# Performance work log

Hardware: AMD Instinct MI355X
Metric: run time of the kernel (lower is better)

The kernel has to match this reference:

```python
import jax, jax.numpy as jnp
import numpy as np

N = 50000      # nodes
E = 800000     # unique directed edges (avg degree 16)
F = 64         # input_dim
D = 64         # output_dim (== F -> residual is identity)
ALPHA = 0.5
LCS_THR = 0.5  # enable_lcs_masking=True, lcs_threshold=0.5


def setup_inputs() -> dict:
    key = jax.random.key(0)
    ks = jax.random.split(key, 16)
    x = jax.random.normal(ks[0], (N, F), jnp.float32)
    src = jax.random.randint(ks[1], (E,), 0, N, jnp.int32)
    dst = jax.random.randint(ks[2], (E,), 0, N, jnp.int32)
    # integer-valued multiplicities in {1,2,3,4} (recurring-transaction counts)
    counts = jnp.floor(jax.random.uniform(ks[3], (E,), jnp.float32) * 4.0) + 1.0
    def lin(k, fan_in, shape):
        return jax.random.normal(k, shape, jnp.float32) / np.float32(np.sqrt(fan_in))
    return dict(
        x=x, counts=counts,
        W_s2d=lin(ks[4], F, (F, D)), b_s2d=jnp.zeros((D,), jnp.float32),
        W_d2s=lin(ks[5], F, (F, D)), b_d2s=jnp.zeros((D,), jnp.float32),
        W_l1=lin(ks[6], 2 * F, (2 * F, F)), b_l1=jnp.zeros((F,), jnp.float32),
        W_l2=lin(ks[7], F, (F, 1)), b_l2=jnp.zeros((1,), jnp.float32),
        W_g1=lin(ks[8], 2 * D, (2 * D, D)), b_g1=jnp.zeros((D,), jnp.float32),
        W_g2=lin(ks[9], D, (D, 1)), b_g2=jnp.zeros((1,), jnp.float32),
        src=src, dst=dst,
    )


def reference(x, counts, W_s2d, b_s2d, W_d2s, b_d2s,
              W_l1, b_l1, W_l2, b_l2, W_g1, b_g1, W_g2, b_g2,
              src, dst):
    # in/out degrees from full (unmasked) multiplicities, clamped at 1
    in_deg = jnp.maximum(jax.ops.segment_sum(counts, dst, num_segments=N), 1.0)
    out_deg = jnp.maximum(jax.ops.segment_sum(counts, src, num_segments=N), 1.0)

    # LCS per unique edge: sigmoid(MLP([x_src, x_dst])), detached in torch
    lcs_in = jnp.concatenate([x[src], x[dst]], axis=-1)          # [E, 2F]
    lcs = jax.nn.sigmoid(
        jax.nn.relu(lcs_in @ W_l1 + b_l1) @ W_l2 + b_l2)[:, 0]   # [E]
    lcs = jax.lax.stop_gradient(lcs)
    keep = (lcs >= LCS_THR).astype(x.dtype)                      # LCS masking

    # symmetric-normalized edge weights with multiplicity counts
    w = counts * keep * jax.lax.rsqrt(out_deg[src] * in_deg[dst])  # [E]

    # direction-aware message passing (redundancy-eliminated, per unique edge)
    h_s2d = x @ W_s2d + b_s2d                                    # [N, D]
    h_d2s = x @ W_d2s + b_d2s                                    # [N, D]
    m_in = jax.ops.segment_sum(w[:, None] * h_s2d[src], dst, num_segments=N)
    m_out = jax.ops.segment_sum(w[:, None] * h_d2s[dst], src, num_segments=N)

    # node-wise gating over inbound vs outbound flows
    gate = jax.nn.sigmoid(
        jax.nn.relu(jnp.concatenate([m_in, m_out], axis=-1) @ W_g1 + b_g1)
        @ W_g2 + b_g2)                                           # [N, 1]

    # gated alpha-blend + identity residual (input_dim == output_dim)
    out = ALPHA * gate * m_in + (1.0 - ALPHA) * (1.0 - gate) * m_out + x
    return out
```

## Files before the change

kernel.cpp:

```cpp
#include <hip/hip_runtime.h>
#include <math.h>


typedef unsigned long long u64;

#define SLOTS 56

__device__ __forceinline__ float bflo(unsigned u) { return __uint_as_float(u << 16); }
__device__ __forceinline__ float bfhi(unsigned u) { return __uint_as_float(u & 0xffff0000u); }
__device__ __forceinline__ unsigned rne16(float f) {
    unsigned u = __float_as_uint(f);
    return (u + 0x7fffu + ((u >> 16) & 1u)) >> 16;
}

__global__ __launch_bounds__(256) void proj_zero_kernel(
    const float* __restrict__ x,
    const float* __restrict__ Wl1,  const float* __restrict__ bl1,
    const float* __restrict__ Ws2d, const float* __restrict__ bs2d,
    const float* __restrict__ Wd2s, const float* __restrict__ bd2s,
    const float* __restrict__ Wg1,  float* __restrict__ Wg1q,
    float* __restrict__ A, float* __restrict__ B,
    unsigned* __restrict__ Ah, unsigned* __restrict__ Bh,
    unsigned* __restrict__ HSh, unsigned* __restrict__ HDh,
    int4* __restrict__ zp4, int nz4, int PB, int N)
{
    if (blockIdx.x >= PB) {
        if (blockIdx.x == PB + 64) {
            for (int i = threadIdx.x; i < 8192; i += 256) {
                const int k = i >> 6, c = i & 63;
                Wg1q[((k >> 2) * 64 + c) * 4 + (k & 3)] = Wg1[i];
            }
            return;
        }
        const int t0 = (blockIdx.x - PB) * 256 + threadIdx.x;
        const int stride = 64 * 256;
        const int4 z = make_int4(0, 0, 0, 0);
        for (int i = t0; i < nz4; i += stride) zp4[i] = z;
        return;
    }
    __shared__ float xs[64][64];
    const int tid  = threadIdx.x;
    const int n0   = blockIdx.x * 64;
    const int wv   = tid >> 6;
    const int cc   = tid & 63;
    const int side = wv & 1;
    const int par  = wv >> 1;

    const float* W0 = side ? (Wl1 + 64 * 64) : Wl1;
    const float* W1 = side ? Wd2s : Ws2d;
    const float  b0 = side ? 0.f : bl1[cc];
    const float  b1 = side ? bd2s[cc] : bs2d[cc];
    float*    oA  = side ? B  : A;
    unsigned* oAh = side ? Bh : Ah;
    unsigned* oH  = side ? HDh : HSh;

    float w0[64], w1[64];
#pragma unroll
    for (int k = 0; k < 64; ++k) {
        w0[k] = W0[k * 64 + cc];
        w1[k] = W1[k * 64 + cc];
    }

#pragma unroll
    for (int j = 0; j < 4; ++j) {
        int f4  = tid + j * 256;
        int row = f4 >> 4;
        int c4  = f4 & 15;
        int gn  = n0 + row;
        float4 v = (gn < N) ? ((const float4*)x)[(long)gn * 16 + c4]
                            : make_float4(0.f, 0.f, 0.f, 0.f);
        ((float4*)&xs[row][0])[c4] = v;
    }
    __syncthreads();

    const int nmax = (N - n0 < 64) ? (N - n0) : 64;
    for (int n = par; n < nmax; n += 2) {
        float a0 = b0, a1 = b1;
#pragma unroll
        for (int k = 0; k < 64; k += 4) {
            float4 xv = *((const float4*)&xs[n][k]);
            a0 += xv.x * w0[k] + xv.y * w0[k + 1] + xv.z * w0[k + 2] + xv.w * w0[k + 3];
            a1 += xv.x * w1[k] + xv.y * w1[k + 1] + xv.z * w1[k + 2] + xv.w * w1[k + 3];
        }
        const long gn = n0 + n;
        oA[gn * 64 + cc] = a0;
        const float p0 = __shfl_xor(a0, 1);
        const float p1 = __shfl_xor(a1, 1);
        if ((cc & 1) == 0) {
            oAh[gn * 32 + (cc >> 1)] = (rne16(p0) << 16) | rne16(a0);
            oH [gn * 32 + (cc >> 1)] = (rne16(p1) << 16) | rne16(a1);
        }
    }
}

#define LCS_MARGIN 0.04f
__global__ __launch_bounds__(256) void edge_w_kernel(
    const int* __restrict__ src, const int* __restrict__ dst,
    const float* __restrict__ counts,
    const float* __restrict__ A, const float* __restrict__ B,
    const unsigned* __restrict__ Ah, const unsigned* __restrict__ Bh,
    const float* __restrict__ Wl2, const float* __restrict__ bl2,
    u64* __restrict__ pk, unsigned* __restrict__ rec, int N, int E)
{
    const int tid = threadIdx.x;
    const int e   = blockIdx.x * 32 + (tid >> 3);
    const int c   = tid & 7;
    if (e >= E) return;

    const int s = src[e];
    const int d = dst[e];
    const uint4  ua  = *((const uint4*)(Ah + (long)s * 32 + c * 4));
    const uint4  ub  = *((const uint4*)(Bh + (long)d * 32 + c * 4));
    const float4 wl0 = *((const float4*)(Wl2 + c * 8));
    const float4 wl1 = *((const float4*)(Wl2 + c * 8 + 4));

    float p = fmaxf(bflo(ua.x) + bflo(ub.x), 0.f) * wl0.x
            + fmaxf(bfhi(ua.x) + bfhi(ub.x), 0.f) * wl0.y
            + fmaxf(bflo(ua.y) + bflo(ub.y), 0.f) * wl0.z
            + fmaxf(bfhi(ua.y) + bfhi(ub.y), 0.f) * wl0.w
            + fmaxf(bflo(ua.z) + bflo(ub.z), 0.f) * wl1.x
            + fmaxf(bfhi(ua.z) + bfhi(ub.z), 0.f) * wl1.y
            + fmaxf(bflo(ua.w) + bflo(ub.w), 0.f) * wl1.z
            + fmaxf(bfhi(ua.w) + bfhi(ub.w), 0.f) * wl1.w;
    p += __shfl_xor(p, 1); p += __shfl_xor(p, 2); p += __shfl_xor(p, 4);

    float z = p + bl2[0];
    if (fabsf(z) < LCS_MARGIN) {
        const float4 a0 = *((const float4*)(A + (long)s * 64 + c * 8));
        const float4 a1 = *((const float4*)(A + (long)s * 64 + c * 8 + 4));
        const float4 b0 = *((const float4*)(B + (long)d * 64 + c * 8));
        const float4 b1 = *((const float4*)(B + (long)d * 64 + c * 8 + 4));
        float q = fmaxf(a0.x + b0.x, 0.f) * wl0.x + fmaxf(a0.y + b0.y, 0.f) * wl0.y
                + fmaxf(a0.z + b0.z, 0.f) * wl0.z + fmaxf(a0.w + b0.w, 0.f) * wl0.w
                + fmaxf(a1.x + b1.x, 0.f) * wl1.x + fmaxf(a1.y + b1.y, 0.f) * wl1.y
                + fmaxf(a1.z + b1.z, 0.f) * wl1.z + fmaxf(a1.w + b1.w, 0.f) * wl1.w;
        q += __shfl_xor(q, 1); q += __shfl_xor(q, 2); q += __shfl_xor(q, 4);
        z = q + bl2[0];
    }

    if (c == 0) {
        const u64 keep = (z >= 0.f) ? 1ull : 0ull;
        const unsigned ic = (unsigned)__float2int_rn(counts[e]);
        const u64 od = atomicAdd(pk + d,     (keep << 32) | (u64)ic);
        const u64 os = atomicAdd(pk + N + s, (keep << 32) | (u64)ic);
        if (keep) {
            rec[(long)d * SLOTS + (int)(od >> 32)]       = ((unsigned)s << 16) | ic;
            rec[(long)(N + s) * SLOTS + (int)(os >> 32)] = ((unsigned)d << 16) | ic;
        }
    }
}

__global__ __launch_bounds__(256) void gather_gate_kernel(
    const u64* __restrict__ pk, const unsigned* __restrict__ rec,
    const unsigned* __restrict__ HSh, const unsigned* __restrict__ HDh,
    const float* __restrict__ x,
    const float* __restrict__ Wg1q, const float* __restrict__ bg1,
    const float* __restrict__ Wg2, const float* __restrict__ bg2,
    float* __restrict__ out, int N)
{
    __shared__ float mbuf[16][128];
    const int tid  = threadIdx.x;
    const int wv   = tid >> 6;
    const int lane = tid & 63;
    const int g    = lane >> 3;
    const int c    = lane & 7;
    const int nb   = blockIdx.x * 16 + wv * 4;

    const unsigned* pklo = (const unsigned*)pk;

    for (int j = 0; j < 4; ++j) {
        const int n   = nb + j;
        const int row = wv * 4 + j;
        if (n >= N) {
            if (g == 0) {
#pragma unroll
                for (int q = 0; q < 8; ++q) {
                    mbuf[row][c * 8 + q]      = 0.f;
                    mbuf[row][64 + c * 8 + q] = 0.f;
                }
            }
            continue;
        }

        const u64 pin  = pk[n];
        const u64 pout = pk[N + n];
        const int ei = (int)(pin >> 32);
        const int eo = (int)(pout >> 32);
        const float qin  = 1.f / sqrtf(fmaxf((float)(unsigned)pin,  1.f));
        const float qout = 1.f / sqrtf(fmaxf((float)(unsigned)pout, 1.f));
        const unsigned* rin  = rec + (long)n * SLOTS;
        const unsigned* rout = rec + (long)(N + n) * SLOTS;

        float mi[8], mo[8];
#pragma unroll
        for (int q = 0; q < 8; ++q) { mi[q] = 0.f; mo[q] = 0.f; }

        int ii = g, jo = g;
        while ((ii < ei) || (jo < eo)) {
            const bool pa = ii < ei;
            const bool pb = jo < eo;
            const unsigned ra = rin[pa ? ii : 0];
            const unsigned rb = rout[pb ? jo : 0];
            const unsigned sa = ra >> 16;
            const unsigned sb = rb >> 16;
            const float dga = (float)pklo[2 * (N + (int)sa)];
            const float dgb = (float)pklo[2 * (int)sb];
            const float wa = pa ? (float)(ra & 0xFFu) * (1.f / sqrtf(fmaxf(dga, 1.f))) : 0.f;
            const float wb = pb ? (float)(rb & 0xFFu) * (1.f / sqrtf(fmaxf(dgb, 1.f))) : 0.f;
            const uint4 ua = *((const uint4*)(HSh + (long)sa * 32 + c * 4));
            const uint4 ub = *((const uint4*)(HDh + (long)sb * 32 + c * 4));
            mi[0] += wa * bflo(ua.x);  mo[0] += wb * bflo(ub.x);
            mi[1] += wa * bfhi(ua.x);  mo[1] += wb * bfhi(ub.x);
            mi[2] += wa * bflo(ua.y);  mo[2] += wb * bflo(ub.y);
            mi[3] += wa * bfhi(ua.y);  mo[3] += wb * bfhi(ub.y);
            mi[4] += wa * bflo(ua.z);  mo[4] += wb * bflo(ub.z);
            mi[5] += wa * bfhi(ua.z);  mo[5] += wb * bfhi(ub.z);
            mi[6] += wa * bflo(ua.w);  mo[6] += wb * bflo(ub.w);
            mi[7] += wa * bfhi(ua.w);  mo[7] += wb * bfhi(ub.w);
            ii += 8; jo += 8;
        }

#pragma unroll
        for (int q = 0; q < 8; ++q) {
            mi[q] += __shfl_xor(mi[q], 8);
            mi[q] += __shfl_xor(mi[q], 16);
            mi[q] += __shfl_xor(mi[q], 32);
            mo[q] += __shfl_xor(mo[q], 8);
            mo[q] += __shfl_xor(mo[q], 16);
            mo[q] += __shfl_xor(mo[q], 32);
        }
        if (g == 0) {
#pragma unroll
            for (int q = 0; q < 8; ++q) {
                mbuf[row][c * 8 + q]      = mi[q] * qin;
                mbuf[row][64 + c * 8 + q] = mo[q] * qout;
            }
        }
    }

    const float bgv = bg1[lane];
    float ac0 = bgv, ac1 = bgv, ac2 = bgv, ac3 = bgv;
    const float* m0 = &mbuf[wv * 4 + 0][0];
    const float* m1 = &mbuf[wv * 4 + 1][0];
    const float* m2 = &mbuf[wv * 4 + 2][0];
    const float* m3 = &mbuf[wv * 4 + 3][0];
#pragma unroll 4
    for (int k4 = 0; k4 < 32; ++k4) {
        const float4 w4 = ((const float4*)Wg1q)[k4 * 64 + lane];
        const float4 q0 = ((const float4*)m0)[k4];
        const float4 q1 = ((const float4*)m1)[k4];
        const float4 q2 = ((const float4*)m2)[k4];
        const float4 q3 = ((const float4*)m3)[k4];
        ac0 += q0.x * w4.x + q0.y * w4.y + q0.z * w4.z + q0.w * w4.w;
        ac1 += q1.x * w4.x + q1.y * w4.y + q1.z * w4.z + q1.w * w4.w;
        ac2 += q2.x * w4.x + q2.y * w4.y + q2.z * w4.z + q2.w * w4.w;
        ac3 += q3.x * w4.x + q3.y * w4.y + q3.z * w4.z + q3.w * w4.w;
    }
    const float wg2 = Wg2[lane];
    float v0 = fmaxf(ac0, 0.f) * wg2;
    float v1 = fmaxf(ac1, 0.f) * wg2;
    float v2 = fmaxf(ac2, 0.f) * wg2;
    float v3 = fmaxf(ac3, 0.f) * wg2;
#pragma unroll
    for (int m = 1; m <= 32; m <<= 1) {
        v0 += __shfl_xor(v0, m);
        v1 += __shfl_xor(v1, m);
        v2 += __shfl_xor(v2, m);
        v3 += __shfl_xor(v3, m);
    }
    const float bb = bg2[0];
    float gt[4];
    gt[0] = 1.f / (1.f + expf(-(v0 + bb)));
    gt[1] = 1.f / (1.f + expf(-(v1 + bb)));
    gt[2] = 1.f / (1.f + expf(-(v2 + bb)));
    gt[3] = 1.f / (1.f + expf(-(v3 + bb)));

#pragma unroll
    for (int j = 0; j < 4; ++j) {
        const int n = nb + j;
        if (n >= N) continue;
        const float miv = mbuf[wv * 4 + j][lane];
        const float mov = mbuf[wv * 4 + j][64 + lane];
        out[(long)n * 64 + lane] = 0.5f * gt[j] * miv + 0.5f * (1.f - gt[j]) * mov
                                 + x[(long)n * 64 + lane];
    }
}

extern "C" void kernel_launch(void* const* d_in, const int* in_sizes, int n_in,
                              void* d_out, int out_size, void* d_ws, size_t ws_size,
                              hipStream_t stream) {
    const float* x      = (const float*)d_in[0];
    const float* counts = (const float*)d_in[1];
    const float* Ws2d   = (const float*)d_in[2];
    const float* bs2d   = (const float*)d_in[3];
    const float* Wd2s   = (const float*)d_in[4];
    const float* bd2s   = (const float*)d_in[5];
    const float* Wl1    = (const float*)d_in[6];
    const float* bl1    = (const float*)d_in[7];
    const float* Wl2    = (const float*)d_in[8];
    const float* bl2    = (const float*)d_in[9];
    const float* Wg1    = (const float*)d_in[10];
    const float* bg1    = (const float*)d_in[11];
    const float* Wg2    = (const float*)d_in[12];
    const float* bg2    = (const float*)d_in[13];
    const int*   src    = (const int*)d_in[14];
    const int*   dst    = (const int*)d_in[15];

    const int N  = in_sizes[0] / 64;
    const int E  = in_sizes[14];
    const int PB = (N + 63) / 64;

    float* ws      = (float*)d_ws;
    float* Wg1q    = ws;
    float* A       = ws + 8192;
    float* B       = A + 64L * N;
    unsigned* Ah   = (unsigned*)(B + 64L * N);
    unsigned* Bh   = Ah + 32L * N;
    unsigned* HSh  = Bh + 32L * N;
    unsigned* HDh  = HSh + 32L * N;
    u64* pk        = (u64*)(HDh + 32L * N);
    unsigned* rec  = (unsigned*)(pk + 2L * N);

    proj_zero_kernel<<<PB + 65, 256, 0, stream>>>(
        x, Wl1, bl1, Ws2d, bs2d, Wd2s, bd2s, Wg1, Wg1q,
        A, B, Ah, Bh, HSh, HDh, (int4*)pk, N, PB, N);

    edge_w_kernel<<<(E + 31) / 32, 256, 0, stream>>>(
        src, dst, counts, A, B, Ah, Bh, Wl2, bl2, pk, rec, N, E);

    gather_gate_kernel<<<(N + 15) / 16, 256, 0, stream>>>(
        pk, rec, HSh, HDh, x, Wg1q, bg1, Wg2, bg2, (float*)d_out, N);
}
```

Before: 277.0 us.

## Fuse three kernels into persistent cooperative megakernel and overlap HS/HD projection with edge pass

Replaces the three launches with one persistent cooperative kernel that uses grid-wide syncs between phases. The HS/HD message projection moves out of the first phase and is interleaved with the edge-scoring tiles, so it overlaps that latency-bound pass. Register weight arrays are halved per tile. Costs: grid syncs, a fixed 1024-block grid under a 4-blocks-per-CU launch bound, and extra x reloads for the second projection pass.

```diff
diff --git a/kernel.cpp b/kernel.cpp
--- a/kernel.cpp
+++ b/kernel.cpp
@@ -1,10 +1,14 @@
 #include <hip/hip_runtime.h>
+#include <hip/hip_cooperative_groups.h>
 #include <math.h>
 
+namespace cg = cooperative_groups;
+
 
 typedef unsigned long long u64;
 
 #define SLOTS 56
+#define LCS_MARGIN 0.04f
 
 __device__ __forceinline__ float bflo(unsigned u) { return __uint_as_float(u << 16); }
 __device__ __forceinline__ float bfhi(unsigned u) { return __uint_as_float(u & 0xffff0000u); }
@@ -13,53 +17,48 @@
     return (u + 0x7fffu + ((u >> 16) & 1u)) >> 16;
 }
 
-__global__ __launch_bounds__(256) void proj_zero_kernel(
-    const float* __restrict__ x,
-    const float* __restrict__ Wl1,  const float* __restrict__ bl1,
-    const float* __restrict__ Ws2d, const float* __restrict__ bs2d,
-    const float* __restrict__ Wd2s, const float* __restrict__ bd2s,
-    const float* __restrict__ Wg1,  float* __restrict__ Wg1q,
-    float* __restrict__ A, float* __restrict__ B,
-    unsigned* __restrict__ Ah, unsigned* __restrict__ Bh,
-    unsigned* __restrict__ HSh, unsigned* __restrict__ HDh,
-    int4* __restrict__ zp4, int nz4, int PB, int N)
+union __align__(16) SMem {
+    float xs[64][64];
+    float mbuf[16][128];
+};
+
+struct MArgs {
+    const float* x; const float* counts;
+    const float* Ws2d; const float* bs2d; const float* Wd2s; const float* bd2s;
+    const float* Wl1;  const float* bl1;  const float* Wl2;  const float* bl2;
+    const float* Wg1;  const float* bg1;  const float* Wg2;  const float* bg2;
+    const int* src; const int* dst;
+    float* Wg1q; float* A; float* B;
+    unsigned* Ah; unsigned* Bh; unsigned* HSh; unsigned* HDh;
+    u64* pk; unsigned* rec; float* out;
+    int PB, EB, GB, N, E, nz4;
+    int mode;
+};
+
+template <bool ABPHASE>
+__device__ __forceinline__ void proj_tile(const MArgs& a, int b, int tid, SMem& sm)
 {
-    if (blockIdx.x >= PB) {
-        if (blockIdx.x == PB + 64) {
-            for (int i = threadIdx.x; i < 8192; i += 256) {
-                const int k = i >> 6, c = i & 63;
-                Wg1q[((k >> 2) * 64 + c) * 4 + (k & 3)] = Wg1[i];
-            }
-            return;
-        }
-        const int t0 = (blockIdx.x - PB) * 256 + threadIdx.x;
-        const int stride = 64 * 256;
-        const int4 z = make_int4(0, 0, 0, 0);
-        for (int i = t0; i < nz4; i += stride) zp4[i] = z;
-        return;
-    }
-    __shared__ float xs[64][64];
-    const int tid  = threadIdx.x;
-    const int n0   = blockIdx.x * 64;
+    const int n0   = b * 64;
     const int wv   = tid >> 6;
     const int cc   = tid & 63;
     const int side = wv & 1;
     const int par  = wv >> 1;
 
-    const float* W0 = side ? (Wl1 + 64 * 64) : Wl1;
-    const float* W1 = side ? Wd2s : Ws2d;
-    const float  b0 = side ? 0.f : bl1[cc];
-    const float  b1 = side ? bd2s[cc] : bs2d[cc];
-    float*    oA  = side ? B  : A;
-    unsigned* oAh = side ? Bh : Ah;
-    unsigned* oH  = side ? HDh : HSh;
-
-    float w0[64], w1[64];
-#pragma unroll
-    for (int k = 0; k < 64; ++k) {
-        w0[k] = W0[k * 64 + cc];
-        w1[k] = W1[k * 64 + cc];
-    }
+    const float* W; float bv; float* oA = nullptr; unsigned* oP;
+    if (ABPHASE) {
+        W  = side ? (a.Wl1 + 64 * 64) : a.Wl1;
+        bv = side ? 0.f : a.bl1[cc];
+        oA = side ? a.B  : a.A;
+        oP = side ? a.Bh : a.Ah;
+    } else {
+        W  = side ? a.Wd2s : a.Ws2d;
+        bv = side ? a.bd2s[cc] : a.bs2d[cc];
+        oP = side ? a.HDh : a.HSh;
+    }
+
+    float w[64];
+#pragma unroll
+    for (int k = 0; k < 64; ++k) w[k] = W[k * 64 + cc];
 
 #pragma unroll
     for (int j = 0; j < 4; ++j) {
@@ -67,52 +66,41 @@
         int row = f4 >> 4;
         int c4  = f4 & 15;
         int gn  = n0 + row;
-        float4 v = (gn < N) ? ((const float4*)x)[(long)gn * 16 + c4]
-                            : make_float4(0.f, 0.f, 0.f, 0.f);
-        ((float4*)&xs[row][0])[c4] = v;
+        float4 v = (gn < a.N) ? ((const float4*)a.x)[(long)gn * 16 + c4]
+                              : make_float4(0.f, 0.f, 0.f, 0.f);
+        ((float4*)&sm.xs[row][0])[c4] = v;
     }
     __syncthreads();
 
-    const int nmax = (N - n0 < 64) ? (N - n0) : 64;
+    const int nmax = (a.N - n0 < 64) ? (a.N - n0) : 64;
     for (int n = par; n < nmax; n += 2) {
-        float a0 = b0, a1 = b1;
+        float acc = bv;
 #pragma unroll
         for (int k = 0; k < 64; k += 4) {
-            float4 xv = *((const float4*)&xs[n][k]);
-            a0 += xv.x * w0[k] + xv.y * w0[k + 1] + xv.z * w0[k + 2] + xv.w * w0[k + 3];
-            a1 += xv.x * w1[k] + xv.y * w1[k + 1] + xv.z * w1[k + 2] + xv.w * w1[k + 3];
+            float4 xv = *((const float4*)&sm.xs[n][k]);
+            acc += xv.x * w[k] + xv.y * w[k + 1] + xv.z * w[k + 2] + xv.w * w[k + 3];
         }
         const long gn = n0 + n;
-        oA[gn * 64 + cc] = a0;
-        const float p0 = __shfl_xor(a0, 1);
-        const float p1 = __shfl_xor(a1, 1);
-        if ((cc & 1) == 0) {
-            oAh[gn * 32 + (cc >> 1)] = (rne16(p0) << 16) | rne16(a0);
-            oH [gn * 32 + (cc >> 1)] = (rne16(p1) << 16) | rne16(a1);
-        }
-    }
-}
-
-#define LCS_MARGIN 0.04f
-__global__ __launch_bounds__(256) void edge_w_kernel(
-    const int* __restrict__ src, const int* __restrict__ dst,
-    const float* __restrict__ counts,
-    const float* __restrict__ A, const float* __restrict__ B,
-    const unsigned* __restrict__ Ah, const unsigned* __restrict__ Bh,
-    const float* __restrict__ Wl2, const float* __restrict__ bl2,
-    u64* __restrict__ pk, unsigned* __restrict__ rec, int N, int E)
+        if (ABPHASE) oA[gn * 64 + cc] = acc;
+        const float p = __shfl_xor(acc, 1);
+        if ((cc & 1) == 0)
+            oP[gn * 32 + (cc >> 1)] = (rne16(p) << 16) | rne16(acc);
+    }
+    __syncthreads();
+}
+
+__device__ __forceinline__ void edge_tile(const MArgs& a, int b, int tid)
 {
-    const int tid = threadIdx.x;
-    const int e   = blockIdx.x * 32 + (tid >> 3);
-    const int c   = tid & 7;
-    if (e >= E) return;
-
-    const int s = src[e];
-    const int d = dst[e];
-    const uint4  ua  = *((const uint4*)(Ah + (long)s * 32 + c * 4));
-    const uint4  ub  = *((const uint4*)(Bh + (long)d * 32 + c * 4));
-    const float4 wl0 = *((const float4*)(Wl2 + c * 8));
-    const float4 wl1 = *((const float4*)(Wl2 + c * 8 + 4));
+    const int e = b * 32 + (tid >> 3);
+    const int c = tid & 7;
+    if (e >= a.E) return;
+
+    const int s = a.src[e];
+    const int d = a.dst[e];
+    const uint4  ua  = *((const uint4*)(a.Ah + (long)s * 32 + c * 4));
+    const uint4  ub  = *((const uint4*)(a.Bh + (long)d * 32 + c * 4));
+    const float4 wl0 = *((const float4*)(a.Wl2 + c * 8));
+    const float4 wl1 = *((const float4*)(a.Wl2 + c * 8 + 4));
 
     float p = fmaxf(bflo(ua.x) + bflo(ub.x), 0.f) * wl0.x
             + fmaxf(bfhi(ua.x) + bfhi(ub.x), 0.f) * wl0.y
@@ -124,49 +112,42 @@
             + fmaxf(bfhi(ua.w) + bfhi(ub.w), 0.f) * wl1.w;
     p += __shfl_xor(p, 1); p += __shfl_xor(p, 2); p += __shfl_xor(p, 4);
 
-    float z = p + bl2[0];
+    float z = p + a.bl2[0];
     if (fabsf(z) < LCS_MARGIN) {
-        const float4 a0 = *((const float4*)(A + (long)s * 64 + c * 8));
-        const float4 a1 = *((const float4*)(A + (long)s * 64 + c * 8 + 4));
-        const float4 b0 = *((const float4*)(B + (long)d * 64 + c * 8));
-        const float4 b1 = *((const float4*)(B + (long)d * 64 + c * 8 + 4));
+        const float4 a0 = *((const float4*)(a.A + (long)s * 64 + c * 8));
+        const float4 a1 = *((const float4*)(a.A + (long)s * 64 + c * 8 + 4));
+        const float4 b0 = *((const float4*)(a.B + (long)d * 64 + c * 8));
+        const float4 b1 = *((const float4*)(a.B + (long)d * 64 + c * 8 + 4));
         float q = fmaxf(a0.x + b0.x, 0.f) * wl0.x + fmaxf(a0.y + b0.y, 0.f) * wl0.y
                 + fmaxf(a0.z + b0.z, 0.f) * wl0.z + fmaxf(a0.w + b0.w, 0.f) * wl0.w
                 + fmaxf(a1.x + b1.x, 0.f) * wl1.x + fmaxf(a1.y + b1.y, 0.f) * wl1.y
                 + fmaxf(a1.z + b1.z, 0.f) * wl1.z + fmaxf(a1.w + b1.w, 0.f) * wl1.w;
         q += __shfl_xor(q, 1); q += __shfl_xor(q, 2); q += __shfl_xor(q, 4);
-        z = q + bl2[0];
+        z = q + a.bl2[0];
     }
 
     if (c == 0) {
         const u64 keep = (z >= 0.f) ? 1ull : 0ull;
-        const unsigned ic = (unsigned)__float2int_rn(counts[e]);
-        const u64 od = atomicAdd(pk + d,     (keep << 32) | (u64)ic);
-        const u64 os = atomicAdd(pk + N + s, (keep << 32) | (u64)ic);
+        const unsigned ic = (unsigned)__float2int_rn(a.counts[e]);
+        const u64 od = atomicAdd(a.pk + d,       (keep << 32) | (u64)ic);
+        const u64 os = atomicAdd(a.pk + a.N + s, (keep << 32) | (u64)ic);
         if (keep) {
-            rec[(long)d * SLOTS + (int)(od >> 32)]       = ((unsigned)s << 16) | ic;
-            rec[(long)(N + s) * SLOTS + (int)(os >> 32)] = ((unsigned)d << 16) | ic;
-        }
-    }
-}
-
-__global__ __launch_bounds__(256) void gather_gate_kernel(
-    const u64* __restrict__ pk, const unsigned* __restrict__ rec,
-    const unsigned* __restrict__ HSh, const unsigned* __restrict__ HDh,
-    const float* __restrict__ x,
-    const float* __restrict__ Wg1q, const float* __restrict__ bg1,
-    const float* __restrict__ Wg2, const float* __restrict__ bg2,
-    float* __restrict__ out, int N)
+            a.rec[(long)d * SLOTS + (int)(od >> 32)]         = ((unsigned)s << 16) | ic;
+            a.rec[(long)(a.N + s) * SLOTS + (int)(os >> 32)] = ((unsigned)d << 16) | ic;
+        }
+    }
+}
+
+__device__ __forceinline__ void gather_tile(const MArgs& a, int b, int tid, SMem& sm)
 {
-    __shared__ float mbuf[16][128];
-    const int tid  = threadIdx.x;
     const int wv   = tid >> 6;
     const int lane = tid & 63;
     const int g    = lane >> 3;
     const int c    = lane & 7;
-    const int nb   = blockIdx.x * 16 + wv * 4;
-
-    const unsigned* pklo = (const unsigned*)pk;
+    const int nb   = b * 16 + wv * 4;
+    const int N    = a.N;
+
+    const unsigned* pklo = (const unsigned*)a.pk;
 
     for (int j = 0; j < 4; ++j) {
         const int n   = nb + j;
@@ -175,21 +156,21 @@
             if (g == 0) {
 #pragma unroll
                 for (int q = 0; q < 8; ++q) {
-                    mbuf[row][c * 8 + q]      = 0.f;
-                    mbuf[row][64 + c * 8 + q] = 0.f;
+                    sm.mbuf[row][c * 8 + q]      = 0.f;
+                    sm.mbuf[row][64 + c * 8 + q] = 0.f;
                 }
             }
             continue;
         }
 
-        const u64 pin  = pk[n];
-        const u64 pout = pk[N + n];
+        const u64 pin  = a.pk[n];
+        const u64 pout = a.pk[N + n];
         const int ei = (int)(pin >> 32);
         const int eo = (int)(pout >> 32);
         const float qin  = 1.f / sqrtf(fmaxf((float)(unsigned)pin,  1.f));
         const float qout = 1.f / sqrtf(fmaxf((float)(unsigned)pout, 1.f));
-        const unsigned* rin  = rec + (long)n * SLOTS;
-        const unsigned* rout = rec + (long)(N + n) * SLOTS;
+        const unsigned* rin  = a.rec + (long)n * SLOTS;
+        const unsigned* rout = a.rec + (long)(N + n) * SLOTS;
 
         float mi[8], mo[8];
 #pragma unroll
@@ -207,8 +188,8 @@
             const float dgb = (float)pklo[2 * (int)sb];
             const float wa = pa ? (float)(ra & 0xFFu) * (1.f / sqrtf(fmaxf(dga, 1.f))) : 0.f;
             const float wb = pb ? (float)(rb & 0xFFu) * (1.f / sqrtf(fmaxf(dgb, 1.f))) : 0.f;
-            const uint4 ua = *((const uint4*)(HSh + (long)sa * 32 + c * 4));
-            const uint4 ub = *((const uint4*)(HDh + (long)sb * 32 + c * 4));
+            const uint4 ua = *((const uint4*)(a.HSh + (long)sa * 32 + c * 4));
+            const uint4 ub = *((const uint4*)(a.HDh + (long)sb * 32 + c * 4));
             mi[0] += wa * bflo(ua.x);  mo[0] += wb * bflo(ub.x);
             mi[1] += wa * bfhi(ua.x);  mo[1] += wb * bfhi(ub.x);
             mi[2] += wa * bflo(ua.y);  mo[2] += wb * bflo(ub.y);
@@ -232,21 +213,21 @@
         if (g == 0) {
 #pragma unroll
             for (int q = 0; q < 8; ++q) {
-                mbuf[row][c * 8 + q]      = mi[q] * qin;
-                mbuf[row][64 + c * 8 + q] = mo[q] * qout;
+                sm.mbuf[row][c * 8 + q]      = mi[q] * qin;
+                sm.mbuf[row][64 + c * 8 + q] = mo[q] * qout;
             }
         }
     }
 
-    const float bgv = bg1[lane];
+    const float bgv = a.bg1[lane];
     float ac0 = bgv, ac1 = bgv, ac2 = bgv, ac3 = bgv;
-    const float* m0 = &mbuf[wv * 4 + 0][0];
-    const float* m1 = &mbuf[wv * 4 + 1][0];
-    const float* m2 = &mbuf[wv * 4 + 2][0];
-    const float* m3 = &mbuf[wv * 4 + 3][0];
+    const float* m0 = &sm.mbuf[wv * 4 + 0][0];
+    const float* m1 = &sm.mbuf[wv * 4 + 1][0];
+    const float* m2 = &sm.mbuf[wv * 4 + 2][0];
+    const float* m3 = &sm.mbuf[wv * 4 + 3][0];
 #pragma unroll 4
     for (int k4 = 0; k4 < 32; ++k4) {
-        const float4 w4 = ((const float4*)Wg1q)[k4 * 64 + lane];
+        const float4 w4 = ((const float4*)a.Wg1q)[k4 * 64 + lane];
         const float4 q0 = ((const float4*)m0)[k4];
         const float4 q1 = ((const float4*)m1)[k4];
         const float4 q2 = ((const float4*)m2)[k4];
@@ -256,7 +237,7 @@
         ac2 += q2.x * w4.x + q2.y * w4.y + q2.z * w4.z + q2.w * w4.w;
         ac3 += q3.x * w4.x + q3.y * w4.y + q3.z * w4.z + q3.w * w4.w;
     }
-    const float wg2 = Wg2[lane];
+    const float wg2 = a.Wg2[lane];
     float v0 = fmaxf(ac0, 0.f) * wg2;
     float v1 = fmaxf(ac1, 0.f) * wg2;
     float v2 = fmaxf(ac2, 0.f) * wg2;
@@ -268,7 +249,7 @@
         v2 += __shfl_xor(v2, m);
         v3 += __shfl_xor(v3, m);
     }
-    const float bb = bg2[0];
+    const float bb = a.bg2[0];
     float gt[4];
     gt[0] = 1.f / (1.f + expf(-(v0 + bb)));
     gt[1] = 1.f / (1.f + expf(-(v1 + bb)));
@@ -279,55 +260,104 @@
     for (int j = 0; j < 4; ++j) {
         const int n = nb + j;
         if (n >= N) continue;
-        const float miv = mbuf[wv * 4 + j][lane];
-        const float mov = mbuf[wv * 4 + j][64 + lane];
-        out[(long)n * 64 + lane] = 0.5f * gt[j] * miv + 0.5f * (1.f - gt[j]) * mov
-                                 + x[(long)n * 64 + lane];
-    }
+        const float miv = sm.mbuf[wv * 4 + j][lane];
+        const float mov = sm.mbuf[wv * 4 + j][64 + lane];
+        a.out[(long)n * 64 + lane] = 0.5f * gt[j] * miv + 0.5f * (1.f - gt[j]) * mov
+                                   + a.x[(long)n * 64 + lane];
+    }
+}
+
+__global__ __launch_bounds__(256, 4) void mega_kernel(MArgs a)
+{
+    __shared__ SMem sm;
+    const int tid = threadIdx.x;
+
+    if (a.mode == 0 || a.mode == 3) {
+        const long t0 = (long)blockIdx.x * 256 + tid;
+        const long gs = (long)gridDim.x * 256;
+        const int4 z = make_int4(0, 0, 0, 0);
+        int4* zp4 = (int4*)a.pk;
+        for (long i = t0; i < a.nz4; i += gs) zp4[i] = z;
+        for (long i = t0; i < 8192; i += gs) {
+            const int k = (int)i >> 6, c = (int)i & 63;
+            a.Wg1q[((k >> 2) * 64 + c) * 4 + (k & 3)] = a.Wg1[(int)i];
+        }
+        for (int b = blockIdx.x; b < a.PB; b += gridDim.x)
+            proj_tile<true>(a, b, tid, sm);
+        if (a.mode == 0) return;
+    }
+
+    if (a.mode == 3) cg::this_grid().sync();
+
+    if (a.mode == 1 || a.mode == 3) {
+        for (int b = blockIdx.x; b < a.EB + a.PB; b += gridDim.x) {
+            if (b < a.EB) edge_tile(a, b, tid);
+            else          proj_tile<false>(a, b - a.EB, tid, sm);
+        }
+        if (a.mode == 1) return;
+    }
+
+    if (a.mode == 3) cg::this_grid().sync();
+
+    for (int b = blockIdx.x; b < a.GB; b += gridDim.x)
+        gather_tile(a, b, tid, sm);
 }
 
 extern "C" void kernel_launch(void* const* d_in, const int* in_sizes, int n_in,
                               void* d_out, int out_size, void* d_ws, size_t ws_size,
                               hipStream_t stream) {
-    const float* x      = (const float*)d_in[0];
-    const float* counts = (const float*)d_in[1];
-    const float* Ws2d   = (const float*)d_in[2];
-    const float* bs2d   = (const float*)d_in[3];
-    const float* Wd2s   = (const float*)d_in[4];
-    const float* bd2s   = (const float*)d_in[5];
-    const float* Wl1    = (const float*)d_in[6];
-    const float* bl1    = (const float*)d_in[7];
-    const float* Wl2    = (const float*)d_in[8];
-    const float* bl2    = (const float*)d_in[9];
-    const float* Wg1    = (const float*)d_in[10];
-    const float* bg1    = (const float*)d_in[11];
-    const float* Wg2    = (const float*)d_in[12];
-    const float* bg2    = (const float*)d_in[13];
-    const int*   src    = (const int*)d_in[14];
-    const int*   dst    = (const int*)d_in[15];
-
-    const int N  = in_sizes[0] / 64;
-    const int E  = in_sizes[14];
-    const int PB = (N + 63) / 64;
-
-    float* ws      = (float*)d_ws;
-    float* Wg1q    = ws;
-    float* A       = ws + 8192;
-    float* B       = A + 64L * N;
-    unsigned* Ah   = (unsigned*)(B + 64L * N);
-    unsigned* Bh   = Ah + 32L * N;
-    unsigned* HSh  = Bh + 32L * N;
-    unsigned* HDh  = HSh + 32L * N;
-    u64* pk        = (u64*)(HDh + 32L * N);
-    unsigned* rec  = (unsigned*)(pk + 2L * N);
-
-    proj_zero_kernel<<<PB + 65, 256, 0, stream>>>(
-        x, Wl1, bl1, Ws2d, bs2d, Wd2s, bd2s, Wg1, Wg1q,
-        A, B, Ah, Bh, HSh, HDh, (int4*)pk, N, PB, N);
-
-    edge_w_kernel<<<(E + 31) / 32, 256, 0, stream>>>(
-        src, dst, counts, A, B, Ah, Bh, Wl2, bl2, pk, rec, N, E);
-
-    gather_gate_kernel<<<(N + 15) / 16, 256, 0, stream>>>(
-        pk, rec, HSh, HDh, x, Wg1q, bg1, Wg2, bg2, (float*)d_out, N);
-}
+    MArgs ha;
+    ha.x      = (const float*)d_in[0];
+    ha.counts = (const float*)d_in[1];
+    ha.Ws2d   = (const float*)d_in[2];
+    ha.bs2d   = (const float*)d_in[3];
+    ha.Wd2s   = (const float*)d_in[4];
+    ha.bd2s   = (const float*)d_in[5];
+    ha.Wl1    = (const float*)d_in[6];
+    ha.bl1    = (const float*)d_in[7];
+    ha.Wl2    = (const float*)d_in[8];
+    ha.bl2    = (const float*)d_in[9];
+    ha.Wg1    = (const float*)d_in[10];
+    ha.bg1    = (const float*)d_in[11];
+    ha.Wg2    = (const float*)d_in[12];
+    ha.bg2    = (const float*)d_in[13];
+    ha.src    = (const int*)d_in[14];
+    ha.dst    = (const int*)d_in[15];
+
+    const int N = in_sizes[0] / 64;
+    const int E = in_sizes[14];
+    ha.N  = N;
+    ha.E  = E;
+    ha.PB = (N + 63) / 64;
+    ha.EB = (E + 31) / 32;
+    ha.GB = (N + 15) / 16;
+    ha.nz4 = N;
+
+    float* ws = (float*)d_ws;
+    ha.Wg1q = ws;
+    ha.A    = ws + 8192;
+    ha.B    = ha.A + 64L * N;
+    ha.Ah   = (unsigned*)(ha.B + 64L * N);
+    ha.Bh   = ha.Ah + 32L * N;
+    ha.HSh  = ha.Bh + 32L * N;
+    ha.HDh  = ha.HSh + 32L * N;
+    ha.pk   = (u64*)(ha.HDh + 32L * N);
+    ha.rec  = (unsigned*)(ha.pk + 2L * N);
+    ha.out  = (float*)d_out;
+
+    const int grid = 1024;
+
+    ha.mode = 3;
+    void* kargs[] = { (void*)&ha };
+    hipError_t err = hipLaunchCooperativeKernel(mega_kernel, dim3(grid),
+                                                dim3(256), kargs, 0, stream);
+    if (err != hipSuccess) {
+        (void)hipGetLastError();
+        MArgs h0 = ha; h0.mode = 0;
+        MArgs h1 = ha; h1.mode = 1;
+        MArgs h2 = ha; h2.mode = 2;
+        hipLaunchKernelGGL(mega_kernel, dim3(grid), dim3(256), 0, stream, h0);
+        hipLaunchKernelGGL(mega_kernel, dim3(grid), dim3(256), 0, stream, h1);
+        hipLaunchKernelGGL(mega_kernel, dim3(grid), dim3(256), 0, stream, h2);
+    }
+}
```

New measurement: 655.1 us. +136.5%, slower.
